# Performance work log

Measured on AMD Instinct MI355X. Metric: run time of the kernel, lower is better.

Reference implementation:

```python
import jax, jax.numpy as jnp
import numpy as np

H = 16  # num heads
DH = 64  # head dim


def setup_inputs() -> dict:
    key = jax.random.key(0)
    ks = jax.random.split(key, 9)
    d = 1024
    s = 0.02
    return {
        "hidden_states": jax.random.normal(ks[0], (16, 1024, d), jnp.float32),
        "Wq": jax.random.normal(ks[1], (d, d), jnp.float32) * s,
        "bq": jax.random.normal(ks[2], (d,), jnp.float32) * s,
        "Wk": jax.random.normal(ks[3], (d, d), jnp.float32) * s,
        "bk": jax.random.normal(ks[4], (d,), jnp.float32) * s,
        "Wv": jax.random.normal(ks[5], (d, d), jnp.float32) * s,
        "bv": jax.random.normal(ks[6], (d,), jnp.float32) * s,
        "Wo": jax.random.normal(ks[7], (d, d), jnp.float32) * s,
        "bo": jax.random.normal(ks[8], (d,), jnp.float32) * s,
    }


def _heads(x):
    b, s, _ = x.shape
    return x.reshape(b, s, H, DH).transpose(0, 2, 1, 3)  # [B,H,S,Dh]


def reference(hidden_states, Wq, bq, Wk, bk, Wv, bv, Wo, bo):
    # torch nn.Linear: y = x @ W.T + b; weights here are [out, in]
    q = _heads(hidden_states @ Wq.T + bq)
    k = _heads(hidden_states @ Wk.T + bk)
    v = _heads(hidden_states @ Wv.T + bv)
    scores = jnp.einsum("bhqd,bhkd->bhqk", q, k) / jnp.sqrt(jnp.float32(DH))
    probs = jax.nn.softmax(scores, axis=-1)
    ctx = jnp.einsum("bhqk,bhkd->bhqd", probs, v)
    b, _, s, _ = ctx.shape
    ctx = ctx.transpose(0, 2, 1, 3).reshape(b, s, H * DH)
    out = ctx @ Wo.T + bo
    # module returns (attention_output, weights=None); return array only
    return out
```

## Files before the change

### kernel.cpp

```cpp
#include <hip/hip_runtime.h>
#include <hip/hip_bf16.h>
#include <stdint.h>


typedef short bf16x8 __attribute__((ext_vector_type(8)));
typedef float f32x4 __attribute__((ext_vector_type(4)));
typedef unsigned short ushort_t;
typedef ushort_t us8 __attribute__((ext_vector_type(8)));

__device__ __forceinline__ ushort_t f2b(float f) {
    unsigned x;
    __builtin_memcpy(&x, &f, 4);
    unsigned r = (x + 0x7fffu + ((x >> 16) & 1u)) >> 16;
    return (ushort_t)r;
}

__device__ __forceinline__ void glds16(const void* g, void* l) {
    __builtin_amdgcn_global_load_lds(
        (const __attribute__((address_space(1))) void*)g,
        (__attribute__((address_space(3))) void*)l, 16, 0, 0);
}

#define MFMA(a, b, c) __builtin_amdgcn_mfma_f32_16x16x32_bf16((a), (b), (c), 0, 0, 0)

__global__ __launch_bounds__(256, 8) void cvt_f32_bf16_kernel(
    const float* __restrict__ in, ushort_t* __restrict__ out, int n8)
{
    int i = blockIdx.x * 256 + threadIdx.x;
    if (i >= n8) return;
    const float4* p = (const float4*)in + (size_t)i * 2;
    float4 a = p[0], b = p[1];
    us8 v;
    v[0] = f2b(a.x); v[1] = f2b(a.y); v[2] = f2b(a.z); v[3] = f2b(a.w);
    v[4] = f2b(b.x); v[5] = f2b(b.y); v[6] = f2b(b.z); v[7] = f2b(b.w);
    *((us8*)out + i) = v;
}

template <bool OUTF>
__global__ __launch_bounds__(256, 2) void gemm_bias_kernel(
    const ushort_t* __restrict__ A,
    const ushort_t* __restrict__ W0, const ushort_t* __restrict__ W1, const ushort_t* __restrict__ W2,
    const float* __restrict__ b0, const float* __restrict__ b1, const float* __restrict__ b2,
    void* __restrict__ C0, void* __restrict__ C1, void* __restrict__ C2,
    int M, int N, int K)
{
    const ushort_t* W = (blockIdx.z == 0) ? W0 : ((blockIdx.z == 1) ? W1 : W2);
    const float* bias = (blockIdx.z == 0) ? b0 : ((blockIdx.z == 1) ? b1 : b2);
    void* C = (blockIdx.z == 0) ? C0 : ((blockIdx.z == 1) ? C1 : C2);

    __shared__ ushort_t As[128 * 64];
    __shared__ ushort_t Bs[128 * 64];

    const int tid = threadIdx.x;
    const int lane = tid & 63;
    const int wave = tid >> 6;
    const int bm = blockIdx.x * 128;
    const int bn = blockIdx.y * 128;
    const int wm = (wave >> 1) * 64;
    const int wn = (wave & 1) * 64;
    const int q = lane >> 4;
    const int ml = lane & 15;

    f32x4 acc[4][4] = {};

    for (int k0 = 0; k0 < K; k0 += 64) {
        __syncthreads();
#pragma unroll
        for (int it = 0; it < 4; ++it) {
            int cid = it * 256 + tid;
            int r = cid >> 3;
            int s = cid & 7;
            int sc = s ^ (r & 7);
            glds16(A + (size_t)(bm + r) * K + k0 + sc * 8, As + cid * 8);
            glds16(W + (size_t)(bn + r) * K + k0 + sc * 8, Bs + cid * 8);
        }
        __syncthreads();
#pragma unroll
        for (int ks = 0; ks < 2; ++ks) {
            bf16x8 af[4], bfr[4];
#pragma unroll
            for (int i = 0; i < 4; ++i) {
                int row = wm + i * 16 + ml;
                int ch = (ks * 4 + q) ^ (row & 7);
                af[i] = *(const bf16x8*)(As + row * 64 + ch * 8);
                int rowb = wn + i * 16 + ml;
                int chb = (ks * 4 + q) ^ (rowb & 7);
                bfr[i] = *(const bf16x8*)(Bs + rowb * 64 + chb * 8);
            }
#pragma unroll
            for (int i = 0; i < 4; ++i)
#pragma unroll
                for (int j = 0; j < 4; ++j)
                    acc[i][j] = MFMA(af[i], bfr[j], acc[i][j]);
        }
    }

#pragma unroll
    for (int j = 0; j < 4; ++j) {
        int col = bn + wn + j * 16 + ml;
        float bv = bias[col];
#pragma unroll
        for (int i = 0; i < 4; ++i) {
            int rowb = bm + wm + i * 16 + q * 4;
#pragma unroll
            for (int r = 0; r < 4; ++r) {
                float v = acc[i][j][r] + bv;
                if (OUTF)
                    ((float*)C)[(size_t)(rowb + r) * N + col] = v;
                else
                    ((ushort_t*)C)[(size_t)(rowb + r) * N + col] = f2b(v);
            }
        }
    }
}

__global__ __launch_bounds__(256, 4) void transpose_v_kernel(
    const ushort_t* __restrict__ V, ushort_t* __restrict__ Vt)
{
    __shared__ ushort_t t[64 * 65];
    const int bh = blockIdx.x;
    const int st = blockIdx.y;
    const int b = bh >> 4, h = bh & 15;
    const int tid = threadIdx.x;

#pragma unroll
    for (int i = 0; i < 16; ++i) {
        int e = i * 256 + tid;
        int s = e >> 6, d = e & 63;
        t[s * 65 + d] = V[(size_t)(b * 1024 + st * 64 + s) * 1024 + h * 64 + d];
    }
    __syncthreads();
#pragma unroll
    for (int i = 0; i < 16; ++i) {
        int e = i * 256 + tid;
        int d = e >> 6, s = e & 63;
        Vt[(size_t)(bh * 64 + d) * 1024 + st * 64 + s] = t[s * 65 + d];
    }
}

__global__ __launch_bounds__(256, 2) void attn_kernel(
    const ushort_t* __restrict__ Q, const ushort_t* __restrict__ K,
    const ushort_t* __restrict__ Vt, ushort_t* __restrict__ ctx)
{
    __shared__ ushort_t Ks[64 * 64];
    __shared__ ushort_t Vs[64 * 64];
    __shared__ ushort_t Ps[4][16 * 72];

    const int bh = blockIdx.x;
    const int qt = blockIdx.y;
    const int b = bh >> 4, h = bh & 15;
    const int tid = threadIdx.x;
    const int lane = tid & 63;
    const int wave = tid >> 6;
    const int q = lane >> 4;
    const int ml = lane & 15;

    bf16x8 qf0, qf1;
    {
        int row = b * 1024 + qt * 64 + wave * 16 + ml;
        const ushort_t* qp = Q + (size_t)row * 1024 + h * 64;
        qf0 = *(const bf16x8*)(qp + q * 8);
        qf1 = *(const bf16x8*)(qp + 32 + q * 8);
    }

    f32x4 o[4] = {};
    float l[4] = {0.f, 0.f, 0.f, 0.f};
    const float cexp = 1.4426950408889634f * 0.125f;

    for (int kt = 0; kt < 16; ++kt) {
        __syncthreads();
#pragma unroll
        for (int it = 0; it < 2; ++it) {
            int cid = it * 256 + tid;
            int r = cid >> 3, s = cid & 7, sc = s ^ (r & 7);
            glds16(K + (size_t)(b * 1024 + kt * 64 + r) * 1024 + h * 64 + sc * 8,
                   Ks + cid * 8);
            glds16(Vt + (size_t)(bh * 64 + r) * 1024 + kt * 64 + sc * 8,
                   Vs + cid * 8);
        }
        __syncthreads();

        f32x4 sacc[4];
#pragma unroll
        for (int n = 0; n < 4; ++n) {
            int row = n * 16 + ml;
            int c0 = q ^ (row & 7);
            int c1 = (4 + q) ^ (row & 7);
            bf16x8 k0 = *(const bf16x8*)(Ks + row * 64 + c0 * 8);
            bf16x8 k1 = *(const bf16x8*)(Ks + row * 64 + c1 * 8);
            f32x4 z = {};
            z = MFMA(qf0, k0, z);
            z = MFMA(qf1, k1, z);
            sacc[n] = z;
        }

        ushort_t* Pw = Ps[wave];
#pragma unroll
        for (int n = 0; n < 4; ++n) {
#pragma unroll
            for (int r = 0; r < 4; ++r) {
                float p = exp2f(sacc[n][r] * cexp);
                l[r] += p;
                Pw[(q * 4 + r) * 72 + n * 16 + ml] = f2b(p);
            }
        }

        bf16x8 pf0 = *(const bf16x8*)(Pw + ml * 72 + q * 8);
        bf16x8 pf1 = *(const bf16x8*)(Pw + ml * 72 + 32 + q * 8);

#pragma unroll
        for (int n = 0; n < 4; ++n) {
            int row = n * 16 + ml;
            int c0 = q ^ (row & 7);
            int c1 = (4 + q) ^ (row & 7);
            bf16x8 v0 = *(const bf16x8*)(Vs + row * 64 + c0 * 8);
            bf16x8 v1 = *(const bf16x8*)(Vs + row * 64 + c1 * 8);
            o[n] = MFMA(pf0, v0, o[n]);
            o[n] = MFMA(pf1, v1, o[n]);
        }
    }

#pragma unroll
    for (int r = 0; r < 4; ++r) {
        float s = l[r];
        s += __shfl_xor(s, 1, 64);
        s += __shfl_xor(s, 2, 64);
        s += __shfl_xor(s, 4, 64);
        s += __shfl_xor(s, 8, 64);
        l[r] = 1.0f / s;
    }

    const int orow = b * 1024 + qt * 64 + wave * 16 + q * 4;
#pragma unroll
    for (int n = 0; n < 4; ++n) {
        int col = h * 64 + n * 16 + ml;
#pragma unroll
        for (int r = 0; r < 4; ++r) {
            ctx[(size_t)(orow + r) * 1024 + col] = f2b(o[n][r] * l[r]);
        }
    }
}

extern "C" void kernel_launch(void* const* d_in, const int* in_sizes, int n_in,
                              void* d_out, int out_size, void* d_ws, size_t ws_size,
                              hipStream_t stream)
{
    const float* X  = (const float*)d_in[0];
    const float* Wq = (const float*)d_in[1];
    const float* bq = (const float*)d_in[2];
    const float* Wk = (const float*)d_in[3];
    const float* bk = (const float*)d_in[4];
    const float* Wv = (const float*)d_in[5];
    const float* bv = (const float*)d_in[6];
    const float* Wo = (const float*)d_in[7];
    const float* bo = (const float*)d_in[8];

    const int D = 1024;
    const int M = in_sizes[0] / D;
    const int Bb = M / 1024;
    const size_t MD = (size_t)M * D;
    const size_t DD = (size_t)D * D;

    ushort_t* ws  = (ushort_t*)d_ws;
    ushort_t* Xbf = ws;
    ushort_t* Qb  = ws + MD;
    ushort_t* Kb  = ws + 2 * MD;
    ushort_t* Vb  = ws + 3 * MD;
    ushort_t* Wqb = ws + 4 * MD;
    ushort_t* Wkb = Wqb + DD;
    ushort_t* Wvb = Wkb + DD;
    ushort_t* Wob = Wvb + DD;
    ushort_t* Vtb = Xbf;
    ushort_t* ctx = Vb;

    dim3 blk(256);

    cvt_f32_bf16_kernel<<<(int)(MD / 8 / 256), blk, 0, stream>>>(X, Xbf, (int)(MD / 8));
    cvt_f32_bf16_kernel<<<(int)(DD / 8 / 256), blk, 0, stream>>>(Wq, Wqb, (int)(DD / 8));
    cvt_f32_bf16_kernel<<<(int)(DD / 8 / 256), blk, 0, stream>>>(Wk, Wkb, (int)(DD / 8));
    cvt_f32_bf16_kernel<<<(int)(DD / 8 / 256), blk, 0, stream>>>(Wv, Wvb, (int)(DD / 8));
    cvt_f32_bf16_kernel<<<(int)(DD / 8 / 256), blk, 0, stream>>>(Wo, Wob, (int)(DD / 8));

    dim3 gqkv(M / 128, D / 128, 3);
    gemm_bias_kernel<false><<<gqkv, blk, 0, stream>>>(Xbf, Wqb, Wkb, Wvb, bq, bk, bv,
                                                      Qb, Kb, Vb, M, D, D);

    transpose_v_kernel<<<dim3(Bb * 16, 16), blk, 0, stream>>>(Vb, Vtb);

    attn_kernel<<<dim3(Bb * 16, 16), blk, 0, stream>>>(Qb, Kb, Vtb, ctx);

    dim3 go(M / 128, D / 128, 1);
    gemm_bias_kernel<true><<<go, blk, 0, stream>>>(ctx, Wob, Wob, Wob, bo, bo, bo,
                                                   d_out, d_out, d_out, M, D, D);
}
```

Measured before the change: 458.9 us.

## Process two query row groups per wave in attention and vectorize P stores

Each wave now handles 32 query rows instead of 16, so every block covers 128 queries and the grid halves. Each K/V tile loaded into LDS is therefore reused across twice as many query rows. The QK MFMA operands are swapped so scores come out transposed. That lets the exponentials be packed into bf16 with perm instructions and written to LDS as 8-byte vector stores instead of scalar stores. The row-sum reduction and normalization are adjusted to this layout. In exchange, register pressure and LDS per block rise, and the bf16 rounding becomes a simpler round-half-up.

```diff
diff --git a/kernel.cpp b/kernel.cpp
--- a/kernel.cpp
+++ b/kernel.cpp
@@ -13,6 +13,11 @@
     __builtin_memcpy(&x, &f, 4);
     unsigned r = (x + 0x7fffu + ((x >> 16) & 1u)) >> 16;
     return (ushort_t)r;
+}
+__device__ __forceinline__ unsigned fbits(float f) {
+    unsigned x;
+    __builtin_memcpy(&x, &f, 4);
+    return x;
 }
 
 __device__ __forceinline__ void glds16(const void* g, void* l) {
@@ -144,7 +149,7 @@
 {
     __shared__ ushort_t Ks[64 * 64];
     __shared__ ushort_t Vs[64 * 64];
-    __shared__ ushort_t Ps[4][16 * 72];
+    __shared__ ushort_t Ps[4][32 * 72];
 
     const int bh = blockIdx.x;
     const int qt = blockIdx.y;
@@ -155,17 +160,20 @@
     const int q = lane >> 4;
     const int ml = lane & 15;
 
-    bf16x8 qf0, qf1;
-    {
-        int row = b * 1024 + qt * 64 + wave * 16 + ml;
+    bf16x8 qf[2][2];
+#pragma unroll
+    for (int mg = 0; mg < 2; ++mg) {
+        int row = b * 1024 + qt * 128 + wave * 32 + mg * 16 + ml;
         const ushort_t* qp = Q + (size_t)row * 1024 + h * 64;
-        qf0 = *(const bf16x8*)(qp + q * 8);
-        qf1 = *(const bf16x8*)(qp + 32 + q * 8);
-    }
-
-    f32x4 o[4] = {};
-    float l[4] = {0.f, 0.f, 0.f, 0.f};
+        qf[mg][0] = *(const bf16x8*)(qp + q * 8);
+        qf[mg][1] = *(const bf16x8*)(qp + 32 + q * 8);
+    }
+
+    f32x4 o[2][4] = {};
+    float l[2] = {0.f, 0.f};
     const float cexp = 1.4426950408889634f * 0.125f;
+
+    ushort_t* Pw = Ps[wave];
 
     for (int kt = 0; kt < 16; ++kt) {
         __syncthreads();
@@ -180,7 +188,6 @@
         }
         __syncthreads();
 
-        f32x4 sacc[4];
 #pragma unroll
         for (int n = 0; n < 4; ++n) {
             int row = n * 16 + ml;
@@ -188,25 +195,31 @@
             int c1 = (4 + q) ^ (row & 7);
             bf16x8 k0 = *(const bf16x8*)(Ks + row * 64 + c0 * 8);
             bf16x8 k1 = *(const bf16x8*)(Ks + row * 64 + c1 * 8);
-            f32x4 z = {};
-            z = MFMA(qf0, k0, z);
-            z = MFMA(qf1, k1, z);
-            sacc[n] = z;
-        }
-
-        ushort_t* Pw = Ps[wave];
-#pragma unroll
-        for (int n = 0; n < 4; ++n) {
-#pragma unroll
-            for (int r = 0; r < 4; ++r) {
-                float p = exp2f(sacc[n][r] * cexp);
-                l[r] += p;
-                Pw[(q * 4 + r) * 72 + n * 16 + ml] = f2b(p);
-            }
-        }
-
-        bf16x8 pf0 = *(const bf16x8*)(Pw + ml * 72 + q * 8);
-        bf16x8 pf1 = *(const bf16x8*)(Pw + ml * 72 + 32 + q * 8);
+#pragma unroll
+            for (int mg = 0; mg < 2; ++mg) {
+                f32x4 z = {};
+                z = MFMA(k0, qf[mg][0], z);
+                z = MFMA(k1, qf[mg][1], z);
+                float p0 = exp2f(z[0] * cexp);
+                float p1 = exp2f(z[1] * cexp);
+                float p2 = exp2f(z[2] * cexp);
+                float p3 = exp2f(z[3] * cexp);
+                l[mg] += (p0 + p1) + (p2 + p3);
+                unsigned d0 = __builtin_amdgcn_perm(fbits(p1) + 0x8000u,
+                                                    fbits(p0) + 0x8000u, 0x07060302u);
+                unsigned d1 = __builtin_amdgcn_perm(fbits(p3) + 0x8000u,
+                                                    fbits(p2) + 0x8000u, 0x07060302u);
+                uint2 dd; dd.x = d0; dd.y = d1;
+                *(uint2*)(Pw + (mg * 16 + ml) * 72 + n * 16 + q * 4) = dd;
+            }
+        }
+
+        bf16x8 pf[2][2];
+#pragma unroll
+        for (int mg = 0; mg < 2; ++mg) {
+            pf[mg][0] = *(const bf16x8*)(Pw + (mg * 16 + ml) * 72 + q * 8);
+            pf[mg][1] = *(const bf16x8*)(Pw + (mg * 16 + ml) * 72 + 32 + q * 8);
+        }
 
 #pragma unroll
         for (int n = 0; n < 4; ++n) {
@@ -215,28 +228,35 @@
             int c1 = (4 + q) ^ (row & 7);
             bf16x8 v0 = *(const bf16x8*)(Vs + row * 64 + c0 * 8);
             bf16x8 v1 = *(const bf16x8*)(Vs + row * 64 + c1 * 8);
-            o[n] = MFMA(pf0, v0, o[n]);
-            o[n] = MFMA(pf1, v1, o[n]);
-        }
-    }
-
-#pragma unroll
-    for (int r = 0; r < 4; ++r) {
-        float s = l[r];
-        s += __shfl_xor(s, 1, 64);
-        s += __shfl_xor(s, 2, 64);
-        s += __shfl_xor(s, 4, 64);
-        s += __shfl_xor(s, 8, 64);
-        l[r] = 1.0f / s;
-    }
-
-    const int orow = b * 1024 + qt * 64 + wave * 16 + q * 4;
-#pragma unroll
-    for (int n = 0; n < 4; ++n) {
-        int col = h * 64 + n * 16 + ml;
+#pragma unroll
+            for (int mg = 0; mg < 2; ++mg) {
+                o[mg][n] = MFMA(pf[mg][0], v0, o[mg][n]);
+                o[mg][n] = MFMA(pf[mg][1], v1, o[mg][n]);
+            }
+        }
+    }
+
+    float li[2];
+#pragma unroll
+    for (int mg = 0; mg < 2; ++mg) {
+        float s = l[mg];
+        s += __shfl_xor(s, 16, 64);
+        s += __shfl_xor(s, 32, 64);
+        li[mg] = 1.0f / s;
+    }
+
+    const int orow_base = b * 1024 + qt * 128 + wave * 32;
+#pragma unroll
+    for (int mg = 0; mg < 2; ++mg) {
 #pragma unroll
         for (int r = 0; r < 4; ++r) {
-            ctx[(size_t)(orow + r) * 1024 + col] = f2b(o[n][r] * l[r]);
+            float lv = __shfl(li[mg], q * 4 + r, 64);
+            int orow = orow_base + mg * 16 + q * 4 + r;
+#pragma unroll
+            for (int n = 0; n < 4; ++n) {
+                ctx[(size_t)orow * 1024 + h * 64 + n * 16 + ml] =
+                    f2b(o[mg][n][r] * lv);
+            }
         }
     }
 }
@@ -287,7 +307,7 @@
 
     transpose_v_kernel<<<dim3(Bb * 16, 16), blk, 0, stream>>>(Vb, Vtb);
 
-    attn_kernel<<<dim3(Bb * 16, 16), blk, 0, stream>>>(Qb, Kb, Vtb, ctx);
+    attn_kernel<<<dim3(Bb * 16, 8), blk, 0, stream>>>(Qb, Kb, Vtb, ctx);
 
     dim3 go(M / 128, D / 128, 1);
     gemm_bias_kernel<true><<<go, blk, 0, stream>>>(ctx, Wob, Wob, Wob, bo, bo, bo,
```

New measurement: 428.3 us. -6.7%, faster.
